# Kernel optimization log

Hardware: AMD Instinct MI355X
Metric: run time of the kernel (lower is better)

Reference implementation:

```python
import jax, jax.numpy as jnp
import numpy as np

N, E = 50000, 800000
IN_DIM, HID, OUT = 128, 128, 2


def _sage_conv(x, src, dst, W_l, W_r, b, num_nodes):
    # PyG SAGEConv (mean aggr): out_i = mean_{j in N(i)} x_j @ W_l + x_i @ W_r + b
    msg_sum = jax.ops.segment_sum(x[src], dst, num_segments=num_nodes)  # [N, d]
    deg = jax.ops.segment_sum(jnp.ones((src.shape[0],), x.dtype), dst, num_segments=num_nodes)
    mean = msg_sum / jnp.maximum(deg, 1.0)[:, None]
    return mean @ W_l + x @ W_r + b


def setup_inputs() -> dict:
    key = jax.random.key(0)
    ks = jax.random.split(key, 9)
    s = lambda fin: 1.0 / np.sqrt(fin)
    x = jax.random.normal(ks[0], (N, IN_DIM), jnp.float32)
    edge_index = jax.random.randint(ks[1], (2, E), 0, N, dtype=jnp.int64)
    W1_l = jax.random.uniform(ks[2], (IN_DIM, HID), jnp.float32, -s(IN_DIM), s(IN_DIM))
    W1_r = jax.random.uniform(ks[3], (IN_DIM, HID), jnp.float32, -s(IN_DIM), s(IN_DIM))
    b1 = jnp.zeros((HID,), jnp.float32)
    W2_l = jax.random.uniform(ks[4], (HID, HID), jnp.float32, -s(HID), s(HID))
    W2_r = jax.random.uniform(ks[5], (HID, HID), jnp.float32, -s(HID), s(HID))
    b2 = jnp.zeros((HID,), jnp.float32)
    W_head = jax.random.uniform(ks[6], (HID, OUT), jnp.float32, -s(HID), s(HID))
    b_head = jax.random.uniform(ks[7], (OUT,), jnp.float32, -s(HID), s(HID))
    return {"x": x, "edge_index": edge_index, "W1_l": W1_l, "W1_r": W1_r, "b1": b1,
            "W2_l": W2_l, "W2_r": W2_r, "b2": b2, "W_head": W_head, "b_head": b_head}


def reference(x, edge_index, W1_l, W1_r, b1, W2_l, W2_r, b2, W_head, b_head):
    num_nodes = x.shape[0]
    src, dst = edge_index[0], edge_index[1]
    h = jax.nn.relu(_sage_conv(x, src, dst, W1_l, W1_r, b1, num_nodes))
    h = jax.nn.relu(_sage_conv(h, src, dst, W2_l, W2_r, b2, num_nodes))
    # dropout is identity in eval mode
    return h @ W_head + b_head
```

## Files before the change

kernel.cpp:

```cpp
#include <hip/hip_runtime.h>
#include <hip/hip_bf16.h>

#define DIM 128
#define CAP 64
#define NB  128
#define NBK 196

typedef short short8_t __attribute__((ext_vector_type(8)));
typedef float float4_t __attribute__((ext_vector_type(4)));
typedef float f32x4 __attribute__((ext_vector_type(4)));
typedef unsigned int u32x2 __attribute__((ext_vector_type(2)));

__device__ __forceinline__ unsigned short f2bf(float f) {
    __hip_bfloat16 h = __float2bfloat16(f);
    return *reinterpret_cast<unsigned short*>(&h);
}
__device__ __forceinline__ float bf2f(unsigned int lo16) {
    return __uint_as_float(lo16 << 16);
}

__global__ __launch_bounds__(1024) void build_hist(
    const int* __restrict__ dst, int* __restrict__ counts,
    const float* __restrict__ x, unsigned short* __restrict__ xB,
    const float* __restrict__ W1l, const float* __restrict__ W1r,
    const float* __restrict__ W2l, const float* __restrict__ W2r,
    unsigned short* __restrict__ Wt1, unsigned short* __restrict__ Wt2,
    int E, int epb, int nx4)
{
    __shared__ int hist[NBK];
    const int b = blockIdx.x;
    const int t = threadIdx.x;
    if (b < NB) {
        for (int j = t; j < NBK; j += 1024) hist[j] = 0;
        __syncthreads();
        const int beg = b * epb;
        const int end = min(beg + epb, E);
        for (int e = beg + t; e < end; e += 1024) {
            int d = __builtin_nontemporal_load(dst + e);
            atomicAdd(&hist[d >> 8], 1);
        }
        __syncthreads();
        for (int j = t; j < NBK; j += 1024) counts[j * NB + b] = hist[j];
        return;
    }
    int idx = (b - NB) * 1024 + t;
    if (idx < nx4) {
        f32x4 v = __builtin_nontemporal_load(reinterpret_cast<const f32x4*>(x) + idx);
        u32x2 p;
        p.x = (unsigned int)f2bf(v.x) | ((unsigned int)f2bf(v.y) << 16);
        p.y = (unsigned int)f2bf(v.z) | ((unsigned int)f2bf(v.w) << 16);
        __builtin_nontemporal_store(p, reinterpret_cast<u32x2*>(xB) + idx);
        return;
    }
    idx -= nx4;
    if (idx < 65536) {
        const int which = idx >> 15;
        const int j = idx & 32767;
        const int c = j >> 8;
        const int k = j & 255;
        const float* Wl = which ? W2l : W1l;
        const float* Wr = which ? W2r : W1r;
        unsigned short* Wt = which ? Wt2 : Wt1;
        float v = (k < DIM) ? Wl[k * DIM + c] : Wr[(k - DIM) * DIM + c];
        Wt[c * 256 + (k ^ ((c & 7) << 3))] = f2bf(v);
    }
}

__global__ __launch_bounds__(1024) void scan_counts(
    int* __restrict__ counts, int* __restrict__ base, int E)
{
    __shared__ int s[256];
    const int t = threadIdx.x;
    int total = 0;
    if (t < NBK) {
        int run = 0;
        for (int i = 0; i < NB; i += 4) {
            int4 c = *reinterpret_cast<int4*>(&counts[t * NB + i]);
            counts[t * NB + i + 0] = run; run += c.x;
            counts[t * NB + i + 1] = run; run += c.y;
            counts[t * NB + i + 2] = run; run += c.z;
            counts[t * NB + i + 3] = run; run += c.w;
        }
        total = run;
    }
    if (t < 256) s[t] = (t < NBK) ? total : 0;
    __syncthreads();
    for (int off = 1; off < 256; off <<= 1) {
        int v = 0;
        if (t < 256 && t >= off) v = s[t - off];
        __syncthreads();
        if (t < 256) s[t] += v;
        __syncthreads();
    }
    if (t < NBK) base[t] = s[t] - total;
    if (t == 0) base[NBK] = E;
}

__global__ __launch_bounds__(1024) void scatter_sorted(
    const int* __restrict__ src, const int* __restrict__ dst,
    const int* __restrict__ counts, const int* __restrict__ base,
    unsigned int* __restrict__ sorted, int E, int epb)
{
    __shared__ int cur[NBK];
    const int b = blockIdx.x;
    const int t = threadIdx.x;
    for (int j = t; j < NBK; j += 1024) cur[j] = base[j] + counts[j * NB + b];
    __syncthreads();
    const int beg = b * epb;
    const int end = min(beg + epb, E);
    for (int e = beg + t; e < end; e += 1024) {
        int d = __builtin_nontemporal_load(dst + e);
        int s = __builtin_nontemporal_load(src + e);
        int pos = atomicAdd(&cur[d >> 8], 1);
        sorted[pos] = ((unsigned int)(d & 255) << 16) | (unsigned int)s;
    }
}

__global__ __launch_bounds__(1024) void build_padded(
    const unsigned int* __restrict__ sorted, const int* __restrict__ base,
    unsigned short* __restrict__ padded, int* __restrict__ deg, int n)
{
    __shared__ int cur[256];
    const int b = blockIdx.x;
    const int t = threadIdx.x;
    if (t < 256) cur[t] = 0;
    __syncthreads();
    const int beg = base[b], end = base[b + 1];
    for (int e = beg + t; e < end; e += 1024) {
        unsigned int v = sorted[e];
        int low = (int)(v >> 16);
        int rank = atomicAdd(&cur[low], 1);
        if (rank < CAP)
            padded[(size_t)(b * 256 + low) * CAP + rank] = (unsigned short)(v & 0xffffu);
    }
    __syncthreads();
    if (t < 256) {
        int node = b * 256 + t;
        if (node < n) deg[node] = cur[t];
    }
}

__global__ __launch_bounds__(256) void gather_mean_bf(
    const unsigned short* __restrict__ xb, const int* __restrict__ deg,
    const unsigned short* __restrict__ padded, unsigned short* __restrict__ mean, int n)
{
    const int node = (blockIdx.x * 256 + threadIdx.x) >> 6;
    const int lane = threadIdx.x & 63;
    if (node >= n) return;
    int len = deg[node];
    if (len > CAP) len = CAP;
    const unsigned short* row = padded + (size_t)node * CAP;
    const int idxreg = (int)row[lane];
    const int row4 = lane >> 4;
    const int col  = lane & 15;
    const uint4* xv = (const uint4*)xb;
    float a0 = 0.f, a1 = 0.f, a2 = 0.f, a3 = 0.f;
    float a4 = 0.f, a5 = 0.f, a6 = 0.f, a7 = 0.f;

#define LOADQ(EOFF)                                                          \
    {                                                                        \
        const int e = (EOFF) + row4;                                         \
        const bool act = e < len;                                            \
        int si = __shfl(idxreg, e, 64);                                      \
        si = act ? si : 0;                                                   \
        uint4 v = xv[(size_t)si * 16 + col];                                 \
        if (!act) { v.x = 0u; v.y = 0u; v.z = 0u; v.w = 0u; }                \
        a0 += bf2f(v.x & 0xffffu); a1 += bf2f(v.x >> 16);                    \
        a2 += bf2f(v.y & 0xffffu); a3 += bf2f(v.y >> 16);                    \
        a4 += bf2f(v.z & 0xffffu); a5 += bf2f(v.z >> 16);                    \
        a6 += bf2f(v.w & 0xffffu); a7 += bf2f(v.w >> 16);                    \
    }

    LOADQ(0) LOADQ(4) LOADQ(8) LOADQ(12)
    if (len > 16) { LOADQ(16) LOADQ(20) LOADQ(24) LOADQ(28) }
    if (len > 32) { LOADQ(32) LOADQ(36) LOADQ(40) LOADQ(44) }
    if (len > 48) { LOADQ(48) LOADQ(52) LOADQ(56) LOADQ(60) }
#undef LOADQ

    a0 += __shfl_xor(a0, 16, 64); a0 += __shfl_xor(a0, 32, 64);
    a1 += __shfl_xor(a1, 16, 64); a1 += __shfl_xor(a1, 32, 64);
    a2 += __shfl_xor(a2, 16, 64); a2 += __shfl_xor(a2, 32, 64);
    a3 += __shfl_xor(a3, 16, 64); a3 += __shfl_xor(a3, 32, 64);
    a4 += __shfl_xor(a4, 16, 64); a4 += __shfl_xor(a4, 32, 64);
    a5 += __shfl_xor(a5, 16, 64); a5 += __shfl_xor(a5, 32, 64);
    a6 += __shfl_xor(a6, 16, 64); a6 += __shfl_xor(a6, 32, 64);
    a7 += __shfl_xor(a7, 16, 64); a7 += __shfl_xor(a7, 32, 64);
    if (row4 == 0) {
        const float r = 1.0f / fmaxf((float)len, 1.0f);
        uint4 o;
        o.x = (unsigned int)f2bf(a0 * r) | ((unsigned int)f2bf(a1 * r) << 16);
        o.y = (unsigned int)f2bf(a2 * r) | ((unsigned int)f2bf(a3 * r) << 16);
        o.z = (unsigned int)f2bf(a4 * r) | ((unsigned int)f2bf(a5 * r) << 16);
        o.w = (unsigned int)f2bf(a6 * r) | ((unsigned int)f2bf(a7 * r) << 16);
        ((uint4*)mean)[(size_t)node * 16 + col] = o;
    }
}

template <bool FUSE_HEAD>
__global__ __launch_bounds__(256, 2) void sage_dense_mfma(
    const unsigned short* __restrict__ meanB, const unsigned short* __restrict__ xinB,
    const unsigned short* __restrict__ WtS,
    const float* __restrict__ bias,
    unsigned short* __restrict__ outB,
    const float* __restrict__ Wh, const float* __restrict__ bh,
    float* __restrict__ outH,
    int n)
{
    __shared__ unsigned short B_s[32768];
    const int t = threadIdx.x;
    const int node0 = blockIdx.x * 64;
    const int wave = t >> 6;
    const int lane = t & 63;
    const int r = lane & 15;
    const int u = lane >> 4;

    int arow = node0 + wave * 16 + r;
    if (arow >= n) arow = n - 1;
    const unsigned short* aM = meanB + (size_t)arow * DIM + u * 8;
    const unsigned short* aX = xinB + (size_t)arow * DIM + u * 8;

    short8_t a[8];
#pragma unroll
    for (int kk = 0; kk < 4; ++kk) {
        a[kk]     = *reinterpret_cast<const short8_t*>(aM + kk * 32);
        a[kk + 4] = *reinterpret_cast<const short8_t*>(aX + kk * 32);
    }

    {
        const uint4* srcp = reinterpret_cast<const uint4*>(WtS);
        uint4* dstp = reinterpret_cast<uint4*>(B_s);
#pragma unroll
        for (int i = 0; i < 16; ++i) dstp[t + i * 256] = srcp[t + i * 256];
    }
    __syncthreads();

    float4_t acc[8];
#pragma unroll
    for (int ft = 0; ft < 8; ++ft) acc[ft] = (float4_t){0.f, 0.f, 0.f, 0.f};

    const int swz = (r & 7) << 3;
#pragma unroll
    for (int kk = 0; kk < 8; ++kk) {
        const int kbase = (kk * 32 + u * 8) ^ swz;
#pragma unroll
        for (int ft = 0; ft < 8; ++ft) {
            const short8_t b = *reinterpret_cast<const short8_t*>(
                &B_s[(ft * 16 + r) * 256 + kbase]);
            acc[ft] = __builtin_amdgcn_mfma_f32_16x16x32_bf16(a[kk], b, acc[ft], 0, 0, 0);
        }
    }

    if (!FUSE_HEAD) {
#pragma unroll
        for (int ft = 0; ft < 8; ++ft) {
            const int feat = ft * 16 + r;
            const float bv = bias[feat];
#pragma unroll
            for (int j = 0; j < 4; ++j) {
                const int node = node0 + wave * 16 + u * 4 + j;
                if (node < n) {
                    outB[(size_t)node * DIM + feat] = f2bf(fmaxf(acc[ft][j] + bv, 0.0f));
                }
            }
        }
    } else {
        float p0[4] = {0.f, 0.f, 0.f, 0.f};
        float p1[4] = {0.f, 0.f, 0.f, 0.f};
#pragma unroll
        for (int ft = 0; ft < 8; ++ft) {
            const int feat = ft * 16 + r;
            const float bv = bias[feat];
            const float w0 = Wh[feat * 2 + 0];
            const float w1 = Wh[feat * 2 + 1];
#pragma unroll
            for (int j = 0; j < 4; ++j) {
                const float h = fmaxf(acc[ft][j] + bv, 0.0f);
                p0[j] += h * w0;
                p1[j] += h * w1;
            }
        }
#pragma unroll
        for (int off = 1; off < 16; off <<= 1) {
#pragma unroll
            for (int j = 0; j < 4; ++j) {
                p0[j] += __shfl_xor(p0[j], off, 64);
                p1[j] += __shfl_xor(p1[j], off, 64);
            }
        }
        if (r == 0) {
            const float bh0 = bh[0], bh1 = bh[1];
#pragma unroll
            for (int j = 0; j < 4; ++j) {
                const int node = node0 + wave * 16 + u * 4 + j;
                if (node < n) {
                    outH[(size_t)node * 2 + 0] = p0[j] + bh0;
                    outH[(size_t)node * 2 + 1] = p1[j] + bh1;
                }
            }
        }
    }
}

extern "C" void kernel_launch(void* const* d_in, const int* in_sizes, int n_in,
                              void* d_out, int out_size, void* d_ws, size_t ws_size,
                              hipStream_t stream) {
    const float* x    = (const float*)d_in[0];
    const int*   ei   = (const int*)d_in[1];
    const float* W1l  = (const float*)d_in[2];
    const float* W1r  = (const float*)d_in[3];
    const float* b1   = (const float*)d_in[4];
    const float* W2l  = (const float*)d_in[5];
    const float* W2r  = (const float*)d_in[6];
    const float* b2   = (const float*)d_in[7];
    const float* Wh   = (const float*)d_in[8];
    const float* bh   = (const float*)d_in[9];
    float* out = (float*)d_out;

    const int n = in_sizes[0] / DIM;
    const int E = in_sizes[1] / 2;
    const int* src = ei;
    const int* dst = ei + E;

    auto align512 = [](size_t v) { return (v + 511) & ~(size_t)511; };
    char* ws = (char*)d_ws;
    size_t off = 0;
    int* deg      = (int*)(ws + off); off = align512(off + (size_t)n * 4);
    int* counts   = (int*)(ws + off); off = align512(off + (size_t)NBK * NB * 4);
    int* base     = (int*)(ws + off); off = align512(off + (size_t)(NBK + 1) * 4);
    unsigned int* sorted = (unsigned int*)(ws + off); off = align512(off + (size_t)E * 4);
    unsigned short* padded = (unsigned short*)(ws + off); off = align512(off + (size_t)n * CAP * 2);
    unsigned short* Wt1 = (unsigned short*)(ws + off); off = align512(off + (size_t)32768 * 2);
    unsigned short* Wt2 = (unsigned short*)(ws + off); off = align512(off + (size_t)32768 * 2);
    unsigned short* xB   = (unsigned short*)(ws + off); off = align512(off + (size_t)n * DIM * 2);
    unsigned short* bufA = (unsigned short*)(ws + off); off = align512(off + (size_t)n * DIM * 2);
    unsigned short* bufB = (unsigned short*)(ws + off); off = align512(off + (size_t)n * DIM * 2);

    const int ggrid = (n + 3) / 4;
    const int mgrid = (n + 63) / 64;

    const int nx4 = n * DIM / 4;
    const int epb = (E + NB - 1) / NB;
    const int hgrid = NB + (nx4 + 65536 + 1023) / 1024;

    build_hist<<<hgrid, 1024, 0, stream>>>(dst, counts, x, xB,
                                           W1l, W1r, W2l, W2r, Wt1, Wt2, E, epb, nx4);
    scan_counts<<<1, 1024, 0, stream>>>(counts, base, E);
    scatter_sorted<<<NB, 1024, 0, stream>>>(src, dst, counts, base, sorted, E, epb);
    build_padded<<<NBK, 1024, 0, stream>>>(sorted, base, padded, deg, n);

    gather_mean_bf<<<ggrid, 256, 0, stream>>>(xB, deg, padded, bufA, n);
    sage_dense_mfma<false><<<mgrid, 256, 0, stream>>>(bufA, xB, Wt1, b1, bufB,
                                                      nullptr, nullptr, nullptr, n);

    gather_mean_bf<<<ggrid, 256, 0, stream>>>(bufB, deg, padded, bufA, n);
    sage_dense_mfma<true><<<mgrid, 256, 0, stream>>>(bufA, bufB, Wt2, b2, nullptr,
                                                     Wh, bh, out, n);
}
```

Measured before the change: 126.5 us.

## Fuse neighbor mean gather into dense SAGE layer and merge scan into scatter

```diff
diff --git a/kernel.cpp b/kernel.cpp
--- a/kernel.cpp
+++ b/kernel.cpp
@@ -66,52 +66,45 @@
     }
 }
 
-__global__ __launch_bounds__(1024) void scan_counts(
-    int* __restrict__ counts, int* __restrict__ base, int E)
+__global__ __launch_bounds__(1024) void scatter_sorted(
+    const int* __restrict__ src, const int* __restrict__ dst,
+    const int* __restrict__ counts, int* __restrict__ base_g,
+    unsigned int* __restrict__ sorted, int E, int epb)
 {
-    __shared__ int s[256];
+    __shared__ int s_tot[256];
+    __shared__ int s_cur[NBK];
+    const int b = blockIdx.x;
     const int t = threadIdx.x;
-    int total = 0;
+
+    int myprefix = 0, total = 0;
     if (t < NBK) {
-        int run = 0;
-        for (int i = 0; i < NB; i += 4) {
-            int4 c = *reinterpret_cast<int4*>(&counts[t * NB + i]);
-            counts[t * NB + i + 0] = run; run += c.x;
-            counts[t * NB + i + 1] = run; run += c.y;
-            counts[t * NB + i + 2] = run; run += c.z;
-            counts[t * NB + i + 3] = run; run += c.w;
-        }
-        total = run;
-    }
-    if (t < 256) s[t] = (t < NBK) ? total : 0;
+        const int* row = &counts[t * NB];
+        for (int i = 0; i < NB; ++i) {
+            int c = row[i];
+            if (i < b) myprefix += c;
+            total += c;
+        }
+    }
+    if (t < 256) s_tot[t] = (t < NBK) ? total : 0;
     __syncthreads();
     for (int off = 1; off < 256; off <<= 1) {
         int v = 0;
-        if (t < 256 && t >= off) v = s[t - off];
-        __syncthreads();
-        if (t < 256) s[t] += v;
-        __syncthreads();
-    }
-    if (t < NBK) base[t] = s[t] - total;
-    if (t == 0) base[NBK] = E;
-}
-
-__global__ __launch_bounds__(1024) void scatter_sorted(
-    const int* __restrict__ src, const int* __restrict__ dst,
-    const int* __restrict__ counts, const int* __restrict__ base,
-    unsigned int* __restrict__ sorted, int E, int epb)
-{
-    __shared__ int cur[NBK];
-    const int b = blockIdx.x;
-    const int t = threadIdx.x;
-    for (int j = t; j < NBK; j += 1024) cur[j] = base[j] + counts[j * NB + b];
-    __syncthreads();
+        if (t < 256 && t >= off) v = s_tot[t - off];
+        __syncthreads();
+        if (t < 256) s_tot[t] += v;
+        __syncthreads();
+    }
+    if (t < NBK) s_cur[t] = (s_tot[t] - total) + myprefix;
+    if (b == 0 && t < NBK) base_g[t] = s_tot[t] - total;
+    if (b == 0 && t == 0) base_g[NBK] = E;
+    __syncthreads();
+
     const int beg = b * epb;
     const int end = min(beg + epb, E);
     for (int e = beg + t; e < end; e += 1024) {
         int d = __builtin_nontemporal_load(dst + e);
         int s = __builtin_nontemporal_load(src + e);
-        int pos = atomicAdd(&cur[d >> 8], 1);
+        int pos = atomicAdd(&s_cur[d >> 8], 1);
         sorted[pos] = ((unsigned int)(d & 255) << 16) | (unsigned int)s;
     }
 }
@@ -140,65 +133,10 @@
     }
 }
 
-__global__ __launch_bounds__(256) void gather_mean_bf(
-    const unsigned short* __restrict__ xb, const int* __restrict__ deg,
-    const unsigned short* __restrict__ padded, unsigned short* __restrict__ mean, int n)
-{
-    const int node = (blockIdx.x * 256 + threadIdx.x) >> 6;
-    const int lane = threadIdx.x & 63;
-    if (node >= n) return;
-    int len = deg[node];
-    if (len > CAP) len = CAP;
-    const unsigned short* row = padded + (size_t)node * CAP;
-    const int idxreg = (int)row[lane];
-    const int row4 = lane >> 4;
-    const int col  = lane & 15;
-    const uint4* xv = (const uint4*)xb;
-    float a0 = 0.f, a1 = 0.f, a2 = 0.f, a3 = 0.f;
-    float a4 = 0.f, a5 = 0.f, a6 = 0.f, a7 = 0.f;
-
-#define LOADQ(EOFF)                                                          \
-    {                                                                        \
-        const int e = (EOFF) + row4;                                         \
-        const bool act = e < len;                                            \
-        int si = __shfl(idxreg, e, 64);                                      \
-        si = act ? si : 0;                                                   \
-        uint4 v = xv[(size_t)si * 16 + col];                                 \
-        if (!act) { v.x = 0u; v.y = 0u; v.z = 0u; v.w = 0u; }                \
-        a0 += bf2f(v.x & 0xffffu); a1 += bf2f(v.x >> 16);                    \
-        a2 += bf2f(v.y & 0xffffu); a3 += bf2f(v.y >> 16);                    \
-        a4 += bf2f(v.z & 0xffffu); a5 += bf2f(v.z >> 16);                    \
-        a6 += bf2f(v.w & 0xffffu); a7 += bf2f(v.w >> 16);                    \
-    }
-
-    LOADQ(0) LOADQ(4) LOADQ(8) LOADQ(12)
-    if (len > 16) { LOADQ(16) LOADQ(20) LOADQ(24) LOADQ(28) }
-    if (len > 32) { LOADQ(32) LOADQ(36) LOADQ(40) LOADQ(44) }
-    if (len > 48) { LOADQ(48) LOADQ(52) LOADQ(56) LOADQ(60) }
-#undef LOADQ
-
-    a0 += __shfl_xor(a0, 16, 64); a0 += __shfl_xor(a0, 32, 64);
-    a1 += __shfl_xor(a1, 16, 64); a1 += __shfl_xor(a1, 32, 64);
-    a2 += __shfl_xor(a2, 16, 64); a2 += __shfl_xor(a2, 32, 64);
-    a3 += __shfl_xor(a3, 16, 64); a3 += __shfl_xor(a3, 32, 64);
-    a4 += __shfl_xor(a4, 16, 64); a4 += __shfl_xor(a4, 32, 64);
-    a5 += __shfl_xor(a5, 16, 64); a5 += __shfl_xor(a5, 32, 64);
-    a6 += __shfl_xor(a6, 16, 64); a6 += __shfl_xor(a6, 32, 64);
-    a7 += __shfl_xor(a7, 16, 64); a7 += __shfl_xor(a7, 32, 64);
-    if (row4 == 0) {
-        const float r = 1.0f / fmaxf((float)len, 1.0f);
-        uint4 o;
-        o.x = (unsigned int)f2bf(a0 * r) | ((unsigned int)f2bf(a1 * r) << 16);
-        o.y = (unsigned int)f2bf(a2 * r) | ((unsigned int)f2bf(a3 * r) << 16);
-        o.z = (unsigned int)f2bf(a4 * r) | ((unsigned int)f2bf(a5 * r) << 16);
-        o.w = (unsigned int)f2bf(a6 * r) | ((unsigned int)f2bf(a7 * r) << 16);
-        ((uint4*)mean)[(size_t)node * 16 + col] = o;
-    }
-}
-
 template <bool FUSE_HEAD>
-__global__ __launch_bounds__(256, 2) void sage_dense_mfma(
-    const unsigned short* __restrict__ meanB, const unsigned short* __restrict__ xinB,
+__global__ __launch_bounds__(256, 3) void sage_layer(
+    const unsigned short* __restrict__ xb,
+    const int* __restrict__ deg, const unsigned short* __restrict__ padded,
     const unsigned short* __restrict__ WtS,
     const float* __restrict__ bias,
     unsigned short* __restrict__ outB,
@@ -206,33 +144,87 @@
     float* __restrict__ outH,
     int n)
 {
-    __shared__ unsigned short B_s[32768];
+    extern __shared__ unsigned short lds[];
+    unsigned short* M_s = lds;
+    unsigned short* B_s = lds + 8192;
+
     const int t = threadIdx.x;
     const int node0 = blockIdx.x * 64;
     const int wave = t >> 6;
     const int lane = t & 63;
     const int r = lane & 15;
     const int u = lane >> 4;
+    const int row4 = lane >> 4;
+    const int col  = lane & 15;
 
     int arow = node0 + wave * 16 + r;
     if (arow >= n) arow = n - 1;
-    const unsigned short* aM = meanB + (size_t)arow * DIM + u * 8;
-    const unsigned short* aX = xinB + (size_t)arow * DIM + u * 8;
-
+    const unsigned short* aX = xb + (size_t)arow * DIM + u * 8;
     short8_t a[8];
 #pragma unroll
-    for (int kk = 0; kk < 4; ++kk) {
-        a[kk]     = *reinterpret_cast<const short8_t*>(aM + kk * 32);
+    for (int kk = 0; kk < 4; ++kk)
         a[kk + 4] = *reinterpret_cast<const short8_t*>(aX + kk * 32);
-    }
+
+    const uint4* xv = (const uint4*)xb;
+#pragma unroll 2
+    for (int nd = 0; nd < 16; ++nd) {
+        const int rowid = wave * 16 + nd;
+        const int node = node0 + rowid;
+        int len = (node < n) ? deg[node] : 0;
+        if (len > CAP) len = CAP;
+        const unsigned short* row = padded + (size_t)node * CAP;
+        const int idxreg = (int)row[lane];
+        float a0 = 0.f, a1 = 0.f, a2 = 0.f, a3 = 0.f;
+        float a4 = 0.f, a5 = 0.f, a6 = 0.f, a7 = 0.f;
+
+#define LOADQ(EOFF)                                                          \
+        {                                                                    \
+            const int e = (EOFF) + row4;                                     \
+            const bool act = e < len;                                        \
+            int si = __shfl(idxreg, e, 64);                                  \
+            si = act ? si : 0;                                               \
+            uint4 v = xv[(size_t)si * 16 + col];                             \
+            if (!act) { v.x = 0u; v.y = 0u; v.z = 0u; v.w = 0u; }            \
+            a0 += bf2f(v.x & 0xffffu); a1 += bf2f(v.x >> 16);                \
+            a2 += bf2f(v.y & 0xffffu); a3 += bf2f(v.y >> 16);                \
+            a4 += bf2f(v.z & 0xffffu); a5 += bf2f(v.z >> 16);                \
+            a6 += bf2f(v.w & 0xffffu); a7 += bf2f(v.w >> 16);                \
+        }
+        LOADQ(0) LOADQ(4) LOADQ(8) LOADQ(12)
+        if (len > 16) { LOADQ(16) LOADQ(20) LOADQ(24) LOADQ(28) }
+        if (len > 32) { LOADQ(32) LOADQ(36) LOADQ(40) LOADQ(44) }
+        if (len > 48) { LOADQ(48) LOADQ(52) LOADQ(56) LOADQ(60) }
+#undef LOADQ
+
+        a0 += __shfl_xor(a0, 16, 64); a0 += __shfl_xor(a0, 32, 64);
+        a1 += __shfl_xor(a1, 16, 64); a1 += __shfl_xor(a1, 32, 64);
+        a2 += __shfl_xor(a2, 16, 64); a2 += __shfl_xor(a2, 32, 64);
+        a3 += __shfl_xor(a3, 16, 64); a3 += __shfl_xor(a3, 32, 64);
+        a4 += __shfl_xor(a4, 16, 64); a4 += __shfl_xor(a4, 32, 64);
+        a5 += __shfl_xor(a5, 16, 64); a5 += __shfl_xor(a5, 32, 64);
+        a6 += __shfl_xor(a6, 16, 64); a6 += __shfl_xor(a6, 32, 64);
+        a7 += __shfl_xor(a7, 16, 64); a7 += __shfl_xor(a7, 32, 64);
+        if (row4 == 0) {
+            const float rcp = 1.0f / fmaxf((float)len, 1.0f);
+            uint4 o;
+            o.x = (unsigned int)f2bf(a0 * rcp) | ((unsigned int)f2bf(a1 * rcp) << 16);
+            o.y = (unsigned int)f2bf(a2 * rcp) | ((unsigned int)f2bf(a3 * rcp) << 16);
+            o.z = (unsigned int)f2bf(a4 * rcp) | ((unsigned int)f2bf(a5 * rcp) << 16);
+            o.w = (unsigned int)f2bf(a6 * rcp) | ((unsigned int)f2bf(a7 * rcp) << 16);
+            *reinterpret_cast<uint4*>((char*)M_s + rowid * 256 +
+                                      ((col * 16) ^ ((rowid & 7) << 4))) = o;
+        }
+    }
+    __syncthreads();
 
     {
-        const uint4* srcp = reinterpret_cast<const uint4*>(WtS);
-        uint4* dstp = reinterpret_cast<uint4*>(B_s);
-#pragma unroll
-        for (int i = 0; i < 16; ++i) dstp[t + i * 256] = srcp[t + i * 256];
-    }
-    __syncthreads();
+        const int rowid = wave * 16 + r;
+        const char* mb = (const char*)M_s + rowid * 256;
+        const int sw = (rowid & 7) << 4;
+#pragma unroll
+        for (int kk = 0; kk < 4; ++kk)
+            a[kk] = *reinterpret_cast<const short8_t*>(mb + ((u * 16 + kk * 64) ^ sw));
+    }
 
     float4_t acc[8];
 #pragma unroll
@@ -240,20 +232,31 @@
 
     const int swz = (r & 7) << 3;
 #pragma unroll
-    for (int kk = 0; kk < 8; ++kk) {
-        const int kbase = (kk * 32 + u * 8) ^ swz;
+    for (int h = 0; h < 2; ++h) {
+        {
+            const uint4* srcp = reinterpret_cast<const uint4*>(WtS) + h * 2048;
+            uint4* dstp = reinterpret_cast<uint4*>(B_s);
+#pragma unroll
+            for (int i = 0; i < 8; ++i) dstp[t + i * 256] = srcp[t + i * 256];
+        }
+        __syncthreads();
+#pragma unroll
+        for (int kk = 0; kk < 8; ++kk) {
+            const int kbase = (kk * 32 + u * 8) ^ swz;
+#pragma unroll
+            for (int fl = 0; fl < 4; ++fl) {
+                const short8_t b = *reinterpret_cast<const short8_t*>(
+                    &B_s[(fl * 16 + r) * 256 + kbase]);
+                acc[h * 4 + fl] = __builtin_amdgcn_mfma_f32_16x16x32_bf16(a[kk], b, acc[h * 4 + fl], 0, 0, 0);
+            }
+        }
+        __syncthreads();
+    }
+
+    if (!FUSE_HEAD) {
 #pragma unroll
         for (int ft = 0; ft < 8; ++ft) {
-            const short8_t b = *reinterpret_cast<const short8_t*>(
-                &B_s[(ft * 16 + r) * 256 + kbase]);
-            acc[ft] = __builtin_amdgcn_mfma_f32_16x16x32_bf16(a[kk], b, acc[ft], 0, 0, 0);
-        }
-    }
-
-    if (!FUSE_HEAD) {
-#pragma unroll
-        for (int ft = 0; ft < 8; ++ft) {
-            const int feat = ft * 16 + r;
+            const int feat = (ft >> 2) * 64 + (ft & 3) * 16 + r;
             const float bv = bias[feat];
 #pragma unroll
             for (int j = 0; j < 4; ++j) {
@@ -268,15 +271,15 @@
         float p1[4] = {0.f, 0.f, 0.f, 0.f};
 #pragma unroll
         for (int ft = 0; ft < 8; ++ft) {
-            const int feat = ft * 16 + r;
+            const int feat = (ft >> 2) * 64 + (ft & 3) * 16 + r;
             const float bv = bias[feat];
             const float w0 = Wh[feat * 2 + 0];
             const float w1 = Wh[feat * 2 + 1];
 #pragma unroll
             for (int j = 0; j < 4; ++j) {
-                const float h = fmaxf(acc[ft][j] + bv, 0.0f);
-                p0[j] += h * w0;
-                p1[j] += h * w1;
+                const float hh = fmaxf(acc[ft][j] + bv, 0.0f);
+                p0[j] += hh * w0;
+                p1[j] += hh * w1;
             }
         }
 #pragma unroll
@@ -328,31 +331,26 @@
     int* counts   = (int*)(ws + off); off = align512(off + (size_t)NBK * NB * 4);
     int* base     = (int*)(ws + off); off = align512(off + (size_t)(NBK + 1) * 4);
     unsigned int* sorted = (unsigned int*)(ws + off); off = align512(off + (size_t)E * 4);
-    unsigned short* padded = (unsigned short*)(ws + off); off = align512(off + (size_t)n * CAP * 2);
+    unsigned short* padded = (unsigned short*)(ws + off);
+    off = align512(off + (size_t)NBK * 256 * CAP * 2);
     unsigned short* Wt1 = (unsigned short*)(ws + off); off = align512(off + (size_t)32768 * 2);
     unsigned short* Wt2 = (unsigned short*)(ws + off); off = align512(off + (size_t)32768 * 2);
     unsigned short* xB   = (unsigned short*)(ws + off); off = align512(off + (size_t)n * DIM * 2);
-    unsigned short* bufA = (unsigned short*)(ws + off); off = align512(off + (size_t)n * DIM * 2);
     unsigned short* bufB = (unsigned short*)(ws + off); off = align512(off + (size_t)n * DIM * 2);
 
-    const int ggrid = (n + 3) / 4;
     const int mgrid = (n + 63) / 64;
-
     const int nx4 = n * DIM / 4;
     const int epb = (E + NB - 1) / NB;
     const int hgrid = NB + (nx4 + 65536 + 1023) / 1024;
+    const size_t lds_bytes = 49152;
 
     build_hist<<<hgrid, 1024, 0, stream>>>(dst, counts, x, xB,
                                            W1l, W1r, W2l, W2r, Wt1, Wt2, E, epb, nx4);
-    scan_counts<<<1, 1024, 0, stream>>>(counts, base, E);
     scatter_sorted<<<NB, 1024, 0, stream>>>(src, dst, counts, base, sorted, E, epb);
     build_padded<<<NBK, 1024, 0, stream>>>(sorted, base, padded, deg, n);
 
-    gather_mean_bf<<<ggrid, 256, 0, stream>>>(xB, deg, padded, bufA, n);
-    sage_dense_mfma<false><<<mgrid, 256, 0, stream>>>(bufA, xB, Wt1, b1, bufB,
-                                                      nullptr, nullptr, nullptr, n);
-
-    gather_mean_bf<<<ggrid, 256, 0, stream>>>(bufB, deg, padded, bufA, n);
-    sage_dense_mfma<true><<<mgrid, 256, 0, stream>>>(bufA, bufB, Wt2, b2, nullptr,
-                                                     Wh, bh, out, n);
-}
+    sage_layer<false><<<mgrid, 256, lds_bytes, stream>>>(xB, deg, padded, Wt1, b1,
+                                                         bufB, nullptr, nullptr, nullptr, n);
+    sage_layer<true><<<mgrid, 256, lds_bytes, stream>>>(bufB, deg, padded, Wt2, b2,
+                                                        nullptr, Wh, bh, out, n);
+}
```

New measurement: 249.2 us. 1.97x slower.
